# Kernel optimization log

Hardware: AMD Instinct MI355X
Metric: run time of the kernel (lower is better)

## Reference

```python
import jax, jax.numpy as jnp
import numpy as np

COLOR_SIZE = 8
FILTERS = 64
LAYERS = 4
CUMSUM_NORM = 256 * 256 * 3  # hardcoded in original: /256/256/3


def setup_inputs() -> dict:
    key = jax.random.key(0)
    k0, k1, k2, k3 = jax.random.split(key, 4)
    s = 0.05
    example = jax.random.randint(k0, (4, 256, 256, 3), 0, COLOR_SIZE, dtype=jnp.int32)
    # per-channel Dense stacks: layer 0 has input dim 1, layers 1..3 have input dim FILTERS
    W_in_first = jax.random.normal(k1, (3, 1, FILTERS), dtype=jnp.float32) * s
    b_in_first = jnp.zeros((3, FILTERS), dtype=jnp.float32)
    W_in_rest = jax.random.normal(k2, (LAYERS - 1, 3, FILTERS, FILTERS), dtype=jnp.float32) * s
    b_in_rest = jnp.zeros((LAYERS - 1, 3, FILTERS), dtype=jnp.float32)
    W_final = jax.random.normal(k3, (3, FILTERS, COLOR_SIZE), dtype=jnp.float32) * s
    b_final = jnp.zeros((3, COLOR_SIZE), dtype=jnp.float32)
    return {
        "example": example,
        "W_in_first": W_in_first, "b_in_first": b_in_first,
        "W_in_rest": W_in_rest, "b_in_rest": b_in_rest,
        "W_final": W_final, "b_final": b_final,
    }


def reference(example, W_in_first, b_in_first, W_in_rest, b_in_rest, W_final, b_final):
    # example: [B, H, W, 3] int in [0, COLOR_SIZE)
    x = example.astype(jnp.float32) / COLOR_SIZE * 2.0 - 1.0
    B, H, W, _ = x.shape
    L = H * W
    x = x.reshape(B, L, 3, 1)

    def layer(x, Wl, bl):
        # per-channel dense + relu: [B, L, 3, din] x [3, din, dout] -> [B, L, 3, dout]
        x = jax.nn.relu(jnp.einsum('blcd,cde->blce', x, Wl) + bl)
        # flatten channels into the sequence and take causal running sum
        x = x.reshape(B, L * 3, FILTERS)
        x = jnp.cumsum(x, axis=-2) / CUMSUM_NORM
        return x.reshape(B, L, 3, FILTERS)

    x = layer(x, W_in_first, b_in_first)
    for i in range(LAYERS - 1):
        x = layer(x, W_in_rest[i], b_in_rest[i])

    # final per-channel dense to color logits (no activation)
    x = jnp.einsum('blcd,cde->blce', x, W_final) + b_final
    return x.reshape(B, H, W, 3, COLOR_SIZE)
```

## Files before the change

kernel.cpp:

```cpp
#include <hip/hip_runtime.h>
#include <stdint.h>


#define BB 4
#define SP 65536
#define SS 196608
#define CI 1024
#define NG 16
#define INVN (1.0f / 196608.0f)

typedef __attribute__((ext_vector_type(8))) _Float16 half8;
typedef __attribute__((ext_vector_type(4))) float    f32x4;

__global__ __launch_bounds__(256)
void prep(const int* __restrict__ ex, const float* __restrict__ W0,
          const float* __restrict__ b0, const float* __restrict__ Wr,
          const float* __restrict__ Wfin,
          _Float16* __restrict__ Wt16, float* __restrict__ Wd32T,
          _Float16* __restrict__ Wf16p,
          float* __restrict__ Wf32, float* __restrict__ tab32,
          int* __restrict__ Hsub, int* __restrict__ Hgrp)
{
    __shared__ int hist[16][24];
    int tid = threadIdx.x, bi = blockIdx.x;
    int b = bi >> 6, g = (bi >> 2) & 15, q = bi & 3;
    for (int i = tid; i < 384; i += 256) hist[i / 24][i % 24] = 0;
    __syncthreads();
    for (int it = 0; it < 4; ++it) {
        int pl = it * 256 + tid;
        const int* ep = ex + ((size_t)b * SP + g * 4096 + q * 1024 + pl) * 3;
        int j = pl >> 6;
        atomicAdd(&hist[j][ep[0]], 1);
        atomicAdd(&hist[j][8 + ep[1]], 1);
        atomicAdd(&hist[j][16 + ep[2]], 1);
    }
    __syncthreads();
    for (int i = tid; i < 384; i += 256) {
        int j = i / 24, cv = i % 24;
        Hsub[(size_t)(b * CI + g * 64 + q * 16 + j) * 24 + cv] = hist[j][cv];
    }
    if (tid < 24) {
        int s = 0;
        for (int j = 0; j < 16; ++j) s += hist[j][tid];
        atomicAdd(&Hgrp[(size_t)(b * NG + g) * 24 + tid], s);
    }
    {
        int i0 = bi * 256 + tid, nth = 256 * 256;
        for (int idx = i0; idx < 36864; idx += nth) {
            int d = idx & 63, f = (idx >> 6) & 63, lc = idx >> 12;
            float v = Wr[(size_t)(lc * 64 + d) * 64 + f];
            Wt16[idx]  = (_Float16)v;
            Wd32T[idx] = v;
        }
        for (int idx = i0; idx < 3072; idx += nth) {
            int d = idx & 63, n = (idx >> 6) & 15, c = idx >> 10;
            Wf16p[idx] = (n < 8) ? (_Float16)Wfin[(size_t)(c * 64 + d) * 8 + n]
                                 : (_Float16)0.f;
        }
        for (int idx = i0; idx < 1536; idx += nth) {
            int d = idx & 63, ck = idx >> 6;
            Wf32[idx] = Wfin[(size_t)((ck >> 3) * 64 + d) * 8 + (ck & 7)];
        }
        for (int idx = i0; idx < 1536; idx += nth) {
            int f = idx & 63, v = (idx >> 6) & 7, c = idx >> 9;
            float xv = v * 0.25f - 1.0f;
            tab32[idx] = fmaxf(W0[c * 64 + f] * xv + b0[c * 64 + f], 0.f);
        }
    }
}

__global__ __launch_bounds__(256, 4)
void midA(const int* __restrict__ ex,
          const int* __restrict__ Hsub, const int* __restrict__ Hgrp,
          const float* __restrict__ tab32,
          const _Float16* __restrict__ W16, const float* __restrict__ WT32,
          const float* __restrict__ bias, _Float16* __restrict__ Y,
          float* __restrict__ A64, float* __restrict__ Ggrp)
{
    __shared__ float stab[1536];
    __shared__ __align__(16) _Float16 bounce[64 * 72];
    __shared__ float segwt[3][4][64];
    __shared__ float basearr[192];
    __shared__ float hpart[4][24];
    __shared__ float carry[64];

    int tid = threadIdx.x, bi = blockIdx.x;
    int b = bi >> 10, ci = bi & 1023, g = ci >> 6, cr = ci & 63;
    int w = tid >> 6, ln = tid & 63, lm = ln & 15, lq = ln >> 4;
    int P0 = ci * 64;

    for (int i = tid; i < 1536; i += 256) stab[i] = tab32[i];
    if (ln < 24) {
        float s = 0.f;
        for (int j = w; j < g; j += 4)
            s += (float)Hgrp[(size_t)(b * NG + j) * 24 + ln];
        const int* hp = Hsub + (size_t)(b * CI + g * 64) * 24 + ln;
        for (int j = w; j < cr; j += 4) s += (float)hp[j * 24];
        hpart[w][ln] = s;
    }
    __syncthreads();

    float y0[3][16];
    {
#pragma unroll
        for (int p = 0; p < 16; ++p) {
            const int* ep = ex + ((size_t)b * SP + P0 + w * 16 + p) * 3;
            y0[0][p] = stab[ep[0] * 64 + ln];
            y0[1][p] = stab[(8 + ep[1]) * 64 + ln];
            y0[2][p] = stab[(16 + ep[2]) * 64 + ln];
        }
#pragma unroll
        for (int c = 0; c < 3; ++c)
#pragma unroll
            for (int p = 1; p < 16; ++p) y0[c][p] += y0[c][p - 1];
#pragma unroll
        for (int c = 0; c < 3; ++c) segwt[c][w][ln] = y0[c][15];
    }
    if (tid < 64) {
        float c0 = 0.f;
#pragma unroll
        for (int cv = 0; cv < 24; ++cv) {
            float cnt = hpart[0][cv] + hpart[1][cv] + hpart[2][cv] + hpart[3][cv];
            c0 += cnt * stab[cv * 64 + tid];
        }
        carry[tid] = c0;
    }
    __syncthreads();

    float off0[3];
#pragma unroll
    for (int c = 0; c < 3; ++c) {
        float o = 0.f;
        for (int w2 = 0; w2 < w; ++w2) o += segwt[c][w2][ln];
        off0[c] = o;
    }
    if (tid < 192) {
        int c = tid >> 6, f = tid & 63;
        const float* wp = WT32 + (size_t)(c * 64 + f) * 64;
        float a = 0.f;
#pragma unroll 16
        for (int d = 0; d < 64; ++d) a += carry[d] * wp[d];
        basearr[tid] = bias[tid] + INVN * a;
    }

    half8 af0[3], af1[3];
#pragma unroll
    for (int c = 0; c < 3; ++c) {
#pragma unroll
        for (int p = 0; p < 16; ++p) {
            float a0 = y0[0][p] + off0[0];
            float a1 = (c >= 1 ? y0[1][p] : (p ? y0[1][p - 1] : 0.f)) + off0[1];
            float a2 = (c == 2 ? y0[2][p] : (p ? y0[2][p - 1] : 0.f)) + off0[2];
            bounce[(w * 16 + p) * 72 + ln] = (_Float16)(a0 + a1 + a2);
        }
        __syncthreads();
        const half8* bb = (const half8*)bounce;
        af0[c] = bb[(w * 16 + lm) * 9 + lq];
        af1[c] = bb[(w * 16 + lm) * 9 + 4 + lq];
        __syncthreads();
    }

    f32x4 acc[3][4];
#pragma unroll
    for (int c = 0; c < 3; ++c)
#pragma unroll
        for (int nt = 0; nt < 4; ++nt) {
            const half8* bp = (const half8*)(W16 + (size_t)(c * 64 + nt * 16 + lm) * 64);
            f32x4 t = {0.f, 0.f, 0.f, 0.f};
            t = __builtin_amdgcn_mfma_f32_16x16x32_f16(af0[c], bp[lq],     t, 0, 0, 0);
            t = __builtin_amdgcn_mfma_f32_16x16x32_f16(af1[c], bp[4 + lq], t, 0, 0, 0);
            acc[c][nt] = t;
        }

    float s[3][4][4], wexcl[3][4];
#pragma unroll
    for (int c = 0; c < 3; ++c)
#pragma unroll
        for (int nt = 0; nt < 4; ++nt) {
            float base = basearr[c * 64 + nt * 16 + lm];
            float run = 0.f;
#pragma unroll
            for (int r = 0; r < 4; ++r) {
                float yv = fmaxf(base + INVN * acc[c][nt][r], 0.f);
                run += yv; s[c][nt][r] = run;
            }
            float v = run;
            float t1 = __shfl_up(v, 16); if (lq >= 1) v += t1;
            float t2 = __shfl_up(v, 32); if (lq >= 2) v += t2;
            wexcl[c][nt] = v - run;
            if (lq == 3) segwt[c][w][nt * 16 + lm] = v;
        }
    __syncthreads();

    float off[3][4];
    {
        float tot[3][4];
#pragma unroll
        for (int c = 0; c < 3; ++c)
#pragma unroll
            for (int nt = 0; nt < 4; ++nt) {
                float o = wexcl[c][nt], ts = 0.f;
#pragma unroll
                for (int w2 = 0; w2 < 4; ++w2) {
                    float wv = segwt[c][w2][nt * 16 + lm];
                    ts += wv;
                    if (w2 < w) o += wv;
                }
                off[c][nt] = o; tot[c][nt] = ts;
            }
        if (w == 0 && lq == 0)
#pragma unroll
            for (int nt = 0; nt < 4; ++nt) {
                float t3 = tot[0][nt] + tot[1][nt] + tot[2][nt];
                A64[(size_t)(b * CI + ci) * 64 + nt * 16 + lm] = t3;
                atomicAdd(&Ggrp[(size_t)(b * NG + g) * 64 + nt * 16 + lm], t3);
            }
    }

#pragma unroll
    for (int c = 0; c < 3; ++c) {
        if (c) __syncthreads();
#pragma unroll
        for (int nt = 0; nt < 4; ++nt) {
            float offT = off[0][nt] + off[1][nt] + off[2][nt];
#pragma unroll
            for (int r = 0; r < 4; ++r) {
                float s1p = r ? s[1][nt][r - 1] : 0.f;
                float s2p = r ? s[2][nt][r - 1] : 0.f;
                float V = offT + s[0][nt][r];
                float ov = (c == 0) ? (V + s1p + s2p)
                         : (c == 1) ? (V + s[1][nt][r] + s2p)
                                    : (V + s[1][nt][r] + s[2][nt][r]);
                bounce[(w * 16 + lq * 4 + r) * 72 + nt * 16 + lm] = (_Float16)ov;
            }
        }
        __syncthreads();
        const half8* bb = (const half8*)bounce;
        _Float16* Yc = Y + ((size_t)(b * 3 + c) * SP + P0) * 64;
#pragma unroll
        for (int q = 0; q < 2; ++q) {
            int idx = q * 256 + tid;
            int pix = idx >> 3, f8 = idx & 7;
            ((half8*)(Yc + (size_t)pix * 64))[f8] = bb[pix * 9 + f8];
        }
    }
}

__global__ __launch_bounds__(256, 4)
void midB(const _Float16* Yin, _Float16* Yout,
          const float* __restrict__ A64p, const float* __restrict__ Ggrp_p,
          const _Float16* __restrict__ W16, const float* __restrict__ WT32,
          const float* __restrict__ bias,
          float* __restrict__ A64, float* __restrict__ Ggrp)
{
    __shared__ __align__(16) _Float16 bounce[64 * 72];
    __shared__ float wtop[3][4][64];
    __shared__ float basearr[192];
    __shared__ float cpart[4][64];
    __shared__ float carry[64];

    int tid = threadIdx.x, bi = blockIdx.x;
    int b = bi >> 10, ci = bi & 1023, g = ci >> 6, cr = ci & 63;
    int w = tid >> 6, ln = tid & 63, lm = ln & 15, lq = ln >> 4;
    int P0 = ci * 64;

    half8 af0[3], af1[3];
#pragma unroll
    for (int c = 0; c < 3; ++c) {
        const half8* ap = (const half8*)(Yin + ((size_t)(b * 3 + c) * SP + P0 + w * 16 + lm) * 64);
        af0[c] = ap[lq]; af1[c] = ap[4 + lq];
    }
    {
        float s = 0.f;
        for (int j = w; j < g; j += 4)
            s += Ggrp_p[(size_t)(b * NG + j) * 64 + ln];
        const float* ap = A64p + (size_t)(b * CI + g * 64) * 64 + ln;
        for (int j = w; j < cr; j += 4) s += ap[j * 64];
        cpart[w][ln] = s;
    }

    f32x4 acc[3][4];
#pragma unroll
    for (int c = 0; c < 3; ++c)
#pragma unroll
        for (int nt = 0; nt < 4; ++nt) {
            const half8* bp = (const half8*)(W16 + (size_t)(c * 64 + nt * 16 + lm) * 64);
            f32x4 t = {0.f, 0.f, 0.f, 0.f};
            t = __builtin_amdgcn_mfma_f32_16x16x32_f16(af0[c], bp[lq],     t, 0, 0, 0);
            t = __builtin_amdgcn_mfma_f32_16x16x32_f16(af1[c], bp[4 + lq], t, 0, 0, 0);
            acc[c][nt] = t;
        }
    __syncthreads();
    if (tid < 64)
        carry[tid] = cpart[0][tid] + cpart[1][tid] + cpart[2][tid] + cpart[3][tid];
    __syncthreads();
    if (tid < 192) {
        int c = tid >> 6, f = tid & 63;
        const float* wp = WT32 + (size_t)(c * 64 + f) * 64;
        float a = 0.f;
#pragma unroll 16
        for (int d = 0; d < 64; ++d) a += carry[d] * wp[d];
        basearr[tid] = bias[tid] + INVN * a;
    }
    __syncthreads();

    float s[3][4][4], wexcl[3][4];
#pragma unroll
    for (int c = 0; c < 3; ++c)
#pragma unroll
        for (int nt = 0; nt < 4; ++nt) {
            float base = basearr[c * 64 + nt * 16 + lm];
            float run = 0.f;
#pragma unroll
            for (int r = 0; r < 4; ++r) {
                float yv = fmaxf(base + INVN * acc[c][nt][r], 0.f);
                run += yv; s[c][nt][r] = run;
            }
            float v = run;
            float t1 = __shfl_up(v, 16); if (lq >= 1) v += t1;
            float t2 = __shfl_up(v, 32); if (lq >= 2) v += t2;
            wexcl[c][nt] = v - run;
            if (lq == 3) wtop[c][w][nt * 16 + lm] = v;
        }
    __syncthreads();

    float off[3][4];
    {
        float tot[3][4];
#pragma unroll
        for (int c = 0; c < 3; ++c)
#pragma unroll
            for (int nt = 0; nt < 4; ++nt) {
                float o = wexcl[c][nt], ts = 0.f;
#pragma unroll
                for (int w2 = 0; w2 < 4; ++w2) {
                    float wv = wtop[c][w2][nt * 16 + lm];
                    ts += wv;
                    if (w2 < w) o += wv;
                }
                off[c][nt] = o; tot[c][nt] = ts;
            }
        if (w == 0 && lq == 0)
#pragma unroll
            for (int nt = 0; nt < 4; ++nt) {
                float t3 = tot[0][nt] + tot[1][nt] + tot[2][nt];
                A64[(size_t)(b * CI + ci) * 64 + nt * 16 + lm] = t3;
                atomicAdd(&Ggrp[(size_t)(b * NG + g) * 64 + nt * 16 + lm], t3);
            }
    }

#pragma unroll
    for (int c = 0; c < 3; ++c) {
        if (c) __syncthreads();
#pragma unroll
        for (int nt = 0; nt < 4; ++nt) {
            float offT = off[0][nt] + off[1][nt] + off[2][nt];
#pragma unroll
            for (int r = 0; r < 4; ++r) {
                float s1p = r ? s[1][nt][r - 1] : 0.f;
                float s2p = r ? s[2][nt][r - 1] : 0.f;
                float V = offT + s[0][nt][r];
                float ov = (c == 0) ? (V + s1p + s2p)
                         : (c == 1) ? (V + s[1][nt][r] + s2p)
                                    : (V + s[1][nt][r] + s[2][nt][r]);
                bounce[(w * 16 + lq * 4 + r) * 72 + nt * 16 + lm] = (_Float16)ov;
            }
        }
        __syncthreads();
        const half8* bb = (const half8*)bounce;
        _Float16* Yc = Yout + ((size_t)(b * 3 + c) * SP + P0) * 64;
#pragma unroll
        for (int q = 0; q < 2; ++q) {
            int idx = q * 256 + tid;
            int pix = idx >> 3, f8 = idx & 7;
            ((half8*)(Yc + (size_t)pix * 64))[f8] = bb[pix * 9 + f8];
        }
    }
}

__global__ __launch_bounds__(256, 4)
void midC(const _Float16* __restrict__ Yin,
          const float* __restrict__ A64p, const float* __restrict__ Ggrp_p,
          const _Float16* __restrict__ W16, const float* __restrict__ WT32,
          const float* __restrict__ bias,
          const _Float16* __restrict__ Wf16p, const float* __restrict__ bfin,
          float* __restrict__ out, float* __restrict__ A64, float* __restrict__ Ggrp)
{
    __shared__ __align__(16) _Float16 bounce[64 * 72];
    __shared__ float wtop[3][4][64];
    __shared__ float basearr[192];
    __shared__ float cpart[4][64];
    __shared__ float carry[64];
    __shared__ __align__(16) float outst[64 * 28];

    int tid = threadIdx.x, bi = blockIdx.x;
    int b = bi >> 10, ci = bi & 1023, g = ci >> 6, cr = ci & 63;
    int w = tid >> 6, ln = tid & 63, lm = ln & 15, lq = ln >> 4;
    int P0 = ci * 64;

    half8 af0[3], af1[3];
#pragma unroll
    for (int c = 0; c < 3; ++c) {
        const half8* ap = (const half8*)(Yin + ((size_t)(b * 3 + c) * SP + P0 + w * 16 + lm) * 64);
        af0[c] = ap[lq]; af1[c] = ap[4 + lq];
    }
    {
        float s = 0.f;
        for (int j = w; j < g; j += 4)
            s += Ggrp_p[(size_t)(b * NG + j) * 64 + ln];
        const float* ap = A64p + (size_t)(b * CI + g * 64) * 64 + ln;
        for (int j = w; j < cr; j += 4) s += ap[j * 64];
        cpart[w][ln] = s;
    }

    f32x4 acc[3][4];
#pragma unroll
    for (int c = 0; c < 3; ++c)
#pragma unroll
        for (int nt = 0; nt < 4; ++nt) {
            const half8* bp = (const half8*)(W16 + (size_t)(c * 64 + nt * 16 + lm) * 64);
            f32x4 t = {0.f, 0.f, 0.f, 0.f};
            t = __builtin_amdgcn_mfma_f32_16x16x32_f16(af0[c], bp[lq],     t, 0, 0, 0);
            t = __builtin_amdgcn_mfma_f32_16x16x32_f16(af1[c], bp[4 + lq], t, 0, 0, 0);
            acc[c][nt] = t;
        }
    __syncthreads();
    if (tid < 64)
        carry[tid] = cpart[0][tid] + cpart[1][tid] + cpart[2][tid] + cpart[3][tid];
    __syncthreads();
    if (tid < 192) {
        int c = tid >> 6, f = tid & 63;
        const float* wp = WT32 + (size_t)(c * 64 + f) * 64;
        float a = 0.f;
#pragma unroll 16
        for (int d = 0; d < 64; ++d) a += carry[d] * wp[d];
        basearr[tid] = bias[tid] + INVN * a;
    }
    __syncthreads();

    float s[3][4][4], wexcl[3][4];
#pragma unroll
    for (int c = 0; c < 3; ++c)
#pragma unroll
        for (int nt = 0; nt < 4; ++nt) {
            float base = basearr[c * 64 + nt * 16 + lm];
            float run = 0.f;
#pragma unroll
            for (int r = 0; r < 4; ++r) {
                float yv = fmaxf(base + INVN * acc[c][nt][r], 0.f);
                run += yv; s[c][nt][r] = run;
            }
            float v = run;
            float t1 = __shfl_up(v, 16); if (lq >= 1) v += t1;
            float t2 = __shfl_up(v, 32); if (lq >= 2) v += t2;
            wexcl[c][nt] = v - run;
            if (lq == 3) wtop[c][w][nt * 16 + lm] = v;
        }
    __syncthreads();

    float off[3][4];
    {
        float tot[3][4];
#pragma unroll
        for (int c = 0; c < 3; ++c)
#pragma unroll
            for (int nt = 0; nt < 4; ++nt) {
                float o = wexcl[c][nt], ts = 0.f;
#pragma unroll
                for (int w2 = 0; w2 < 4; ++w2) {
                    float wv = wtop[c][w2][nt * 16 + lm];
                    ts += wv;
                    if (w2 < w) o += wv;
                }
                off[c][nt] = o; tot[c][nt] = ts;
            }
        if (w == 0 && lq == 0)
#pragma unroll
            for (int nt = 0; nt < 4; ++nt) {
                float t3 = tot[0][nt] + tot[1][nt] + tot[2][nt];
                A64[(size_t)(b * CI + ci) * 64 + nt * 16 + lm] = t3;
                atomicAdd(&Ggrp[(size_t)(b * NG + g) * 64 + nt * 16 + lm], t3);
            }
    }

#pragma unroll
    for (int c = 0; c < 3; ++c) {
        if (c) __syncthreads();
#pragma unroll
        for (int nt = 0; nt < 4; ++nt) {
            float offT = off[0][nt] + off[1][nt] + off[2][nt];
#pragma unroll
            for (int r = 0; r < 4; ++r) {
                float s1p = r ? s[1][nt][r - 1] : 0.f;
                float s2p = r ? s[2][nt][r - 1] : 0.f;
                float V = offT + s[0][nt][r];
                float ov = (c == 0) ? (V + s1p + s2p)
                         : (c == 1) ? (V + s[1][nt][r] + s2p)
                                    : (V + s[1][nt][r] + s[2][nt][r]);
                bounce[(w * 16 + lq * 4 + r) * 72 + nt * 16 + lm] = (_Float16)ov;
            }
        }
        __syncthreads();
        const half8* bb = (const half8*)bounce;
        half8 fa0 = bb[(w * 16 + lm) * 9 + lq];
        half8 fa1 = bb[(w * 16 + lm) * 9 + 4 + lq];
        const half8* fb = (const half8*)(Wf16p + (size_t)(c * 16 + lm) * 64);
        f32x4 t = {0.f, 0.f, 0.f, 0.f};
        t = __builtin_amdgcn_mfma_f32_16x16x32_f16(fa0, fb[lq],     t, 0, 0, 0);
        t = __builtin_amdgcn_mfma_f32_16x16x32_f16(fa1, fb[4 + lq], t, 0, 0, 0);
        if (lm < 8) {
            float bz = bfin[c * 8 + lm];
#pragma unroll
            for (int r = 0; r < 4; ++r)
                outst[(w * 16 + lq * 4 + r) * 28 + c * 8 + lm] = bz + INVN * t[r];
        }
    }
    __syncthreads();
    {
        float4* obase = (float4*)(out + ((size_t)b * SS + (size_t)P0 * 3) * 8);
#pragma unroll
        for (int k = 0; k < 2; ++k) {
            int idx = k * 256 + tid;
            if (idx < 384) {
                int pix = idx / 6, sub = (idx % 6) * 4;
                obase[idx] = *(const float4*)&outst[pix * 28 + sub];
            }
        }
    }
}

__global__ __launch_bounds__(256, 4)
void fixk(const float* __restrict__ A64p, const float* __restrict__ Ggrp_p,
          const float* __restrict__ Wf32, float* __restrict__ out)
{
    __shared__ float cpart[4][64];
    __shared__ float carry[64];
    __shared__ float part[24][8];
    __shared__ float vfix[24];
    int tid = threadIdx.x, bi = blockIdx.x;
    int b = bi >> 10, ci = bi & 1023, g = ci >> 6, cr = ci & 63;
    int w = tid >> 6, ln = tid & 63;
    int P0 = ci * 64;

    {
        float s = 0.f;
        for (int j = w; j < g; j += 4)
            s += Ggrp_p[(size_t)(b * NG + j) * 64 + ln];
        const float* ap = A64p + (size_t)(b * CI + g * 64) * 64 + ln;
        for (int j = w; j < cr; j += 4) s += ap[j * 64];
        cpart[w][ln] = s;
    }
    __syncthreads();
    if (tid < 64)
        carry[tid] = cpart[0][tid] + cpart[1][tid] + cpart[2][tid] + cpart[3][tid];
    __syncthreads();
    if (tid < 192) {
        int ck = tid >> 3, sg = tid & 7;
        const float* wp = Wf32 + ck * 64 + sg * 8;
        const float* cp = carry + sg * 8;
        float vf = 0.f;
#pragma unroll
        for (int d = 0; d < 8; ++d) vf += cp[d] * wp[d];
        part[ck][sg] = vf;
    }
    __syncthreads();
    if (tid < 24) {
        float vf = 0.f;
#pragma unroll
        for (int j = 0; j < 8; ++j) vf += part[tid][j];
        vfix[tid] = INVN * vf;
    }
    __syncthreads();
    float4* obase = (float4*)(out + ((size_t)b * SS + (size_t)P0 * 3) * 8);
#pragma unroll
    for (int k = 0; k < 2; ++k) {
        int idx = k * 256 + tid;
        if (idx < 384) {
            int sub = (idx % 6) * 4;
            float4 v = obase[idx];
            v.x += vfix[sub];
            v.y += vfix[sub + 1];
            v.z += vfix[sub + 2];
            v.w += vfix[sub + 3];
            obase[idx] = v;
        }
    }
}

extern "C" void kernel_launch(void* const* d_in, const int* in_sizes, int n_in,
                              void* d_out, int out_size, void* d_ws, size_t ws_size,
                              hipStream_t stream)
{
    const int*   ex   = (const int*)d_in[0];
    const float* W0   = (const float*)d_in[1];
    const float* b0   = (const float*)d_in[2];
    const float* Wr   = (const float*)d_in[3];
    const float* br   = (const float*)d_in[4];
    const float* Wfin = (const float*)d_in[5];
    const float* bfin = (const float*)d_in[6];
    float* out = (float*)d_out;

    char* ws = (char*)d_ws;
    size_t off = 0;
    _Float16* Y = (_Float16*)(ws + off); off += (size_t)BB * 3 * SP * 64 * 2;
    float* Ggrp1 = (float*)(ws + off); off += (size_t)BB * NG * 64 * 4;
    float* Ggrp2 = (float*)(ws + off); off += (size_t)BB * NG * 64 * 4;
    float* Ggrp3 = (float*)(ws + off); off += (size_t)BB * NG * 64 * 4;
    float* A64_1 = (float*)(ws + off); off += (size_t)BB * CI * 64 * 4;
    float* A64_2 = (float*)(ws + off); off += (size_t)BB * CI * 64 * 4;
    float* A64_3 = (float*)(ws + off); off += (size_t)BB * CI * 64 * 4;
    int* Hsub = (int*)(ws + off); off += (size_t)BB * CI * 24 * 4;
    int* Hgrp = (int*)(ws + off); off += (size_t)BB * NG * 24 * 4;
    _Float16* Wt16  = (_Float16*)(ws + off); off += 36864 * 2;
    float* Wd32T = (float*)(ws + off); off += 36864 * 4;
    _Float16* Wf16p = (_Float16*)(ws + off); off += 3072 * 2;
    float* Wf32  = (float*)(ws + off); off += 1536 * 4;
    float* tab32 = (float*)(ws + off); off += 1536 * 4;

    hipMemsetAsync(Ggrp1, 0, 3 * (size_t)BB * NG * 64 * 4, stream);
    hipMemsetAsync(Hgrp, 0, (size_t)BB * NG * 24 * 4, stream);
    prep<<<256, 256, 0, stream>>>(ex, W0, b0, Wr, Wfin,
                                  Wt16, Wd32T, Wf16p, Wf32, tab32, Hsub, Hgrp);
    midA<<<4096, 256, 0, stream>>>(ex, Hsub, Hgrp, tab32,
                                   Wt16, Wd32T, br, Y, A64_1, Ggrp1);
    midB<<<4096, 256, 0, stream>>>(Y, Y, A64_1, Ggrp1,
                                   Wt16 + 12288, Wd32T + 12288, br + 192,
                                   A64_2, Ggrp2);
    midC<<<4096, 256, 0, stream>>>(Y, A64_2, Ggrp2,
                                   Wt16 + 24576, Wd32T + 24576, br + 384,
                                   Wf16p, bfin, out, A64_3, Ggrp3);
    fixk<<<4096, 256, 0, stream>>>(A64_3, Ggrp3, Wf32, out);
}
```

Measured before the change: 402.5 us.

## Give each wave its own 64-pixel chunk in midB/midC and batch midA bounce writes

```diff
diff --git a/kernel.cpp b/kernel.cpp
--- a/kernel.cpp
+++ b/kernel.cpp
@@ -11,6 +11,12 @@
 
 typedef __attribute__((ext_vector_type(8))) _Float16 half8;
 typedef __attribute__((ext_vector_type(4))) float    f32x4;
+
+#define WAVE_FENCE() do {                                    \
+    __builtin_amdgcn_sched_barrier(0);                       \
+    asm volatile("s_waitcnt lgkmcnt(0)" ::: "memory");       \
+    __builtin_amdgcn_sched_barrier(0);                       \
+} while (0)
 
 __global__ __launch_bounds__(256)
 void prep(const int* __restrict__ ex, const float* __restrict__ W0,
@@ -78,7 +84,7 @@
           float* __restrict__ A64, float* __restrict__ Ggrp)
 {
     __shared__ float stab[1536];
-    __shared__ __align__(16) _Float16 bounce[64 * 72];
+    __shared__ __align__(16) _Float16 bounce3[3][64 * 72];
     __shared__ float segwt[3][4][64];
     __shared__ float basearr[192];
     __shared__ float hpart[4][24];
@@ -127,12 +133,24 @@
     }
     __syncthreads();
 
-    float off0[3];
-#pragma unroll
-    for (int c = 0; c < 3; ++c) {
-        float o = 0.f;
-        for (int w2 = 0; w2 < w; ++w2) o += segwt[c][w2][ln];
-        off0[c] = o;
+    {
+        float off0[3];
+#pragma unroll
+        for (int c = 0; c < 3; ++c) {
+            float o = 0.f;
+            for (int w2 = 0; w2 < w; ++w2) o += segwt[c][w2][ln];
+            off0[c] = o;
+        }
+#pragma unroll
+        for (int p = 0; p < 16; ++p) {
+            float S0 = y0[0][p] + off0[0], S1 = y0[1][p] + off0[1], S2 = y0[2][p] + off0[2];
+            float P1 = p ? y0[1][p - 1] + off0[1] : off0[1];
+            float P2 = p ? y0[2][p - 1] + off0[2] : off0[2];
+            int row = w * 16 + p;
+            bounce3[0][row * 72 + ln] = (_Float16)(S0 + P1 + P2);
+            bounce3[1][row * 72 + ln] = (_Float16)(S0 + S1 + P2);
+            bounce3[2][row * 72 + ln] = (_Float16)(S0 + S1 + S2);
+        }
     }
     if (tid < 192) {
         int c = tid >> 6, f = tid & 63;
@@ -142,35 +160,23 @@
         for (int d = 0; d < 64; ++d) a += carry[d] * wp[d];
         basearr[tid] = bias[tid] + INVN * a;
     }
-
-    half8 af0[3], af1[3];
+    __syncthreads();
+
+    f32x4 acc[3][4];
 #pragma unroll
     for (int c = 0; c < 3; ++c) {
-#pragma unroll
-        for (int p = 0; p < 16; ++p) {
-            float a0 = y0[0][p] + off0[0];
-            float a1 = (c >= 1 ? y0[1][p] : (p ? y0[1][p - 1] : 0.f)) + off0[1];
-            float a2 = (c == 2 ? y0[2][p] : (p ? y0[2][p - 1] : 0.f)) + off0[2];
-            bounce[(w * 16 + p) * 72 + ln] = (_Float16)(a0 + a1 + a2);
-        }
-        __syncthreads();
-        const half8* bb = (const half8*)bounce;
-        af0[c] = bb[(w * 16 + lm) * 9 + lq];
-        af1[c] = bb[(w * 16 + lm) * 9 + 4 + lq];
-        __syncthreads();
-    }
-
-    f32x4 acc[3][4];
-#pragma unroll
-    for (int c = 0; c < 3; ++c)
+        const half8* bb = (const half8*)&bounce3[c][0];
+        half8 a0 = bb[(w * 16 + lm) * 9 + lq];
+        half8 a1 = bb[(w * 16 + lm) * 9 + 4 + lq];
 #pragma unroll
         for (int nt = 0; nt < 4; ++nt) {
             const half8* bp = (const half8*)(W16 + (size_t)(c * 64 + nt * 16 + lm) * 64);
             f32x4 t = {0.f, 0.f, 0.f, 0.f};
-            t = __builtin_amdgcn_mfma_f32_16x16x32_f16(af0[c], bp[lq],     t, 0, 0, 0);
-            t = __builtin_amdgcn_mfma_f32_16x16x32_f16(af1[c], bp[4 + lq], t, 0, 0, 0);
+            t = __builtin_amdgcn_mfma_f32_16x16x32_f16(a0, bp[lq],     t, 0, 0, 0);
+            t = __builtin_amdgcn_mfma_f32_16x16x32_f16(a1, bp[4 + lq], t, 0, 0, 0);
             acc[c][nt] = t;
         }
+    }
 
     float s[3][4][4], wexcl[3][4];
 #pragma unroll
@@ -192,9 +198,8 @@
         }
     __syncthreads();
 
-    float off[3][4];
-    {
-        float tot[3][4];
+    {
+        float off[3][4], tot[3][4];
 #pragma unroll
         for (int c = 0; c < 3; ++c)
 #pragma unroll
@@ -215,167 +220,168 @@
                 A64[(size_t)(b * CI + ci) * 64 + nt * 16 + lm] = t3;
                 atomicAdd(&Ggrp[(size_t)(b * NG + g) * 64 + nt * 16 + lm], t3);
             }
-    }
-
-#pragma unroll
-    for (int c = 0; c < 3; ++c) {
-        if (c) __syncthreads();
-#pragma unroll
-        for (int nt = 0; nt < 4; ++nt) {
-            float offT = off[0][nt] + off[1][nt] + off[2][nt];
+#pragma unroll
+        for (int nt = 0; nt < 4; ++nt)
 #pragma unroll
             for (int r = 0; r < 4; ++r) {
-                float s1p = r ? s[1][nt][r - 1] : 0.f;
-                float s2p = r ? s[2][nt][r - 1] : 0.f;
-                float V = offT + s[0][nt][r];
-                float ov = (c == 0) ? (V + s1p + s2p)
-                         : (c == 1) ? (V + s[1][nt][r] + s2p)
-                                    : (V + s[1][nt][r] + s[2][nt][r]);
-                bounce[(w * 16 + lq * 4 + r) * 72 + nt * 16 + lm] = (_Float16)ov;
-            }
-        }
-        __syncthreads();
-        const half8* bb = (const half8*)bounce;
-        _Float16* Yc = Y + ((size_t)(b * 3 + c) * SP + P0) * 64;
-#pragma unroll
-        for (int q = 0; q < 2; ++q) {
-            int idx = q * 256 + tid;
-            int pix = idx >> 3, f8 = idx & 7;
-            ((half8*)(Yc + (size_t)pix * 64))[f8] = bb[pix * 9 + f8];
-        }
+                float S0 = off[0][nt] + s[0][nt][r];
+                float S1 = off[1][nt] + s[1][nt][r];
+                float S2 = off[2][nt] + s[2][nt][r];
+                float P1 = off[1][nt] + (r ? s[1][nt][r - 1] : 0.f);
+                float P2 = off[2][nt] + (r ? s[2][nt][r - 1] : 0.f);
+                int row = w * 16 + lq * 4 + r;
+                bounce3[0][row * 72 + nt * 16 + lm] = (_Float16)(S0 + P1 + P2);
+                bounce3[1][row * 72 + nt * 16 + lm] = (_Float16)(S0 + S1 + P2);
+                bounce3[2][row * 72 + nt * 16 + lm] = (_Float16)(S0 + S1 + S2);
+            }
+    }
+    __syncthreads();
+#pragma unroll
+    for (int q = 0; q < 6; ++q) {
+        int idx = q * 256 + tid;
+        int c = idx >> 9, rem = idx & 511;
+        int pix = rem >> 3, f8 = rem & 7;
+        half8 v = *(const half8*)&bounce3[c][pix * 72 + f8 * 8];
+        ((half8*)(Y + ((size_t)(b * 3 + c) * SP + P0 + pix) * 64))[f8] = v;
     }
 }
 
 __global__ __launch_bounds__(256, 4)
-void midB(const _Float16* Yin, _Float16* Yout,
+void midB(const _Float16* __restrict__ Yin, _Float16* __restrict__ Yout,
           const float* __restrict__ A64p, const float* __restrict__ Ggrp_p,
           const _Float16* __restrict__ W16, const float* __restrict__ WT32,
           const float* __restrict__ bias,
           float* __restrict__ A64, float* __restrict__ Ggrp)
 {
-    __shared__ __align__(16) _Float16 bounce[64 * 72];
-    __shared__ float wtop[3][4][64];
-    __shared__ float basearr[192];
     __shared__ float cpart[4][64];
-    __shared__ float carry[64];
+    __shared__ float carry4[4][64];
+    __shared__ float basearr4[4][192];
+    __shared__ __align__(16) _Float16 wb[4][16 * 72];
 
     int tid = threadIdx.x, bi = blockIdx.x;
-    int b = bi >> 10, ci = bi & 1023, g = ci >> 6, cr = ci & 63;
+    int b = bi >> 8, cb = bi & 255;
+    int ci0 = cb * 4, g = cb >> 4, cr0 = ci0 & 63;
     int w = tid >> 6, ln = tid & 63, lm = ln & 15, lq = ln >> 4;
+    int ci = ci0 + w;
     int P0 = ci * 64;
 
-    half8 af0[3], af1[3];
-#pragma unroll
-    for (int c = 0; c < 3; ++c) {
-        const half8* ap = (const half8*)(Yin + ((size_t)(b * 3 + c) * SP + P0 + w * 16 + lm) * 64);
-        af0[c] = ap[lq]; af1[c] = ap[4 + lq];
-    }
     {
         float s = 0.f;
         for (int j = w; j < g; j += 4)
             s += Ggrp_p[(size_t)(b * NG + j) * 64 + ln];
         const float* ap = A64p + (size_t)(b * CI + g * 64) * 64 + ln;
-        for (int j = w; j < cr; j += 4) s += ap[j * 64];
+        for (int j = w; j < cr0; j += 4) s += ap[j * 64];
         cpart[w][ln] = s;
     }
-
-    f32x4 acc[3][4];
-#pragma unroll
-    for (int c = 0; c < 3; ++c)
-#pragma unroll
-        for (int nt = 0; nt < 4; ++nt) {
-            const half8* bp = (const half8*)(W16 + (size_t)(c * 64 + nt * 16 + lm) * 64);
-            f32x4 t = {0.f, 0.f, 0.f, 0.f};
-            t = __builtin_amdgcn_mfma_f32_16x16x32_f16(af0[c], bp[lq],     t, 0, 0, 0);
-            t = __builtin_amdgcn_mfma_f32_16x16x32_f16(af1[c], bp[4 + lq], t, 0, 0, 0);
-            acc[c][nt] = t;
-        }
-    __syncthreads();
-    if (tid < 64)
-        carry[tid] = cpart[0][tid] + cpart[1][tid] + cpart[2][tid] + cpart[3][tid];
+    __syncthreads();
+    {
+        float cw = cpart[0][ln] + cpart[1][ln] + cpart[2][ln] + cpart[3][ln];
+        const float* ap = A64p + (size_t)(b * CI + ci0) * 64 + ln;
+        for (int t = 0; t < w; ++t) cw += ap[t * 64];
+        carry4[w][ln] = cw;
+    }
     __syncthreads();
     if (tid < 192) {
         int c = tid >> 6, f = tid & 63;
         const float* wp = WT32 + (size_t)(c * 64 + f) * 64;
-        float a = 0.f;
-#pragma unroll 16
-        for (int d = 0; d < 64; ++d) a += carry[d] * wp[d];
-        basearr[tid] = bias[tid] + INVN * a;
-    }
-    __syncthreads();
-
-    float s[3][4][4], wexcl[3][4];
+        float a0 = 0.f, a1 = 0.f, a2 = 0.f, a3 = 0.f;
+#pragma unroll 8
+        for (int d = 0; d < 64; ++d) {
+            float wv = wp[d];
+            a0 += carry4[0][d] * wv; a1 += carry4[1][d] * wv;
+            a2 += carry4[2][d] * wv; a3 += carry4[3][d] * wv;
+        }
+        float bz = bias[tid];
+        basearr4[0][tid] = bz + INVN * a0;
+        basearr4[1][tid] = bz + INVN * a1;
+        basearr4[2][tid] = bz + INVN * a2;
+        basearr4[3][tid] = bz + INVN * a3;
+    }
+    __syncthreads();
+
+    float bse[3][4];
 #pragma unroll
     for (int c = 0; c < 3; ++c)
 #pragma unroll
+        for (int nt = 0; nt < 4; ++nt)
+            bse[c][nt] = basearr4[w][c * 64 + nt * 16 + lm];
+    float roff[3][4] = {{0.f,0.f,0.f,0.f},{0.f,0.f,0.f,0.f},{0.f,0.f,0.f,0.f}};
+    _Float16* wbw = &wb[w][0];
+
+#pragma unroll
+    for (int pq = 0; pq < 4; ++pq) {
+        half8 af0[3], af1[3];
+#pragma unroll
+        for (int c = 0; c < 3; ++c) {
+            const half8* ap = (const half8*)(Yin +
+                ((size_t)(b * 3 + c) * SP + P0 + pq * 16 + lm) * 64);
+            af0[c] = ap[lq]; af1[c] = ap[4 + lq];
+        }
+        f32x4 acc[3][4];
+#pragma unroll
+        for (int c = 0; c < 3; ++c)
+#pragma unroll
+            for (int nt = 0; nt < 4; ++nt) {
+                const half8* bp = (const half8*)(W16 + (size_t)(c * 64 + nt * 16 + lm) * 64);
+                f32x4 t = {0.f, 0.f, 0.f, 0.f};
+                t = __builtin_amdgcn_mfma_f32_16x16x32_f16(af0[c], bp[lq],     t, 0, 0, 0);
+                t = __builtin_amdgcn_mfma_f32_16x16x32_f16(af1[c], bp[4 + lq], t, 0, 0, 0);
+                acc[c][nt] = t;
+            }
+
+        float s[3][4][4], off[3][4];
+#pragma unroll
+        for (int c = 0; c < 3; ++c)
+#pragma unroll
+            for (int nt = 0; nt < 4; ++nt) {
+                float base = bse[c][nt];
+                float run = 0.f;
+#pragma unroll
+                for (int r = 0; r < 4; ++r) {
+                    float yv = fmaxf(base + INVN * acc[c][nt][r], 0.f);
+                    run += yv; s[c][nt][r] = run;
+                }
+                float v = run;
+                float t1 = __shfl_up(v, 16); if (lq >= 1) v += t1;
+                float t2 = __shfl_up(v, 32); if (lq >= 2) v += t2;
+                off[c][nt] = roff[c][nt] + (v - run);
+                roff[c][nt] += __shfl(v, 48 + lm);
+            }
+
+#pragma unroll
+        for (int c = 0; c < 3; ++c) {
+#pragma unroll
+            for (int nt = 0; nt < 4; ++nt) {
+                float offT = off[0][nt] + off[1][nt] + off[2][nt];
+#pragma unroll
+                for (int r = 0; r < 4; ++r) {
+                    float s1p = r ? s[1][nt][r - 1] : 0.f;
+                    float s2p = r ? s[2][nt][r - 1] : 0.f;
+                    float V = offT + s[0][nt][r];
+                    float ov = (c == 0) ? (V + s1p + s2p)
+                             : (c == 1) ? (V + s[1][nt][r] + s2p)
+                                        : (V + s[1][nt][r] + s[2][nt][r]);
+                    wbw[(lq * 4 + r) * 72 + nt * 16 + lm] = (_Float16)ov;
+                }
+            }
+            WAVE_FENCE();
+            const half8* bb = (const half8*)wbw;
+            _Float16* Yc = Yout + ((size_t)(b * 3 + c) * SP + P0 + pq * 16) * 64;
+#pragma unroll
+            for (int q = 0; q < 2; ++q) {
+                int idx = q * 64 + ln, pix = idx >> 3, f8 = idx & 7;
+                ((half8*)(Yc + (size_t)pix * 64))[f8] = bb[pix * 9 + f8];
+            }
+        }
+    }
+
+    if (lq == 0)
+#pragma unroll
         for (int nt = 0; nt < 4; ++nt) {
-            float base = basearr[c * 64 + nt * 16 + lm];
-            float run = 0.f;
-#pragma unroll
-            for (int r = 0; r < 4; ++r) {
-                float yv = fmaxf(base + INVN * acc[c][nt][r], 0.f);
-                run += yv; s[c][nt][r] = run;
-            }
-            float v = run;
-            float t1 = __shfl_up(v, 16); if (lq >= 1) v += t1;
-            float t2 = __shfl_up(v, 32); if (lq >= 2) v += t2;
-            wexcl[c][nt] = v - run;
-            if (lq == 3) wtop[c][w][nt * 16 + lm] = v;
-        }
-    __syncthreads();
-
-    float off[3][4];
-    {
-        float tot[3][4];
-#pragma unroll
-        for (int c = 0; c < 3; ++c)
-#pragma unroll
-            for (int nt = 0; nt < 4; ++nt) {
-                float o = wexcl[c][nt], ts = 0.f;
-#pragma unroll
-                for (int w2 = 0; w2 < 4; ++w2) {
-                    float wv = wtop[c][w2][nt * 16 + lm];
-                    ts += wv;
-                    if (w2 < w) o += wv;
-                }
-                off[c][nt] = o; tot[c][nt] = ts;
-            }
-        if (w == 0 && lq == 0)
-#pragma unroll
-            for (int nt = 0; nt < 4; ++nt) {
-                float t3 = tot[0][nt] + tot[1][nt] + tot[2][nt];
-                A64[(size_t)(b * CI + ci) * 64 + nt * 16 + lm] = t3;
-                atomicAdd(&Ggrp[(size_t)(b * NG + g) * 64 + nt * 16 + lm], t3);
-            }
-    }
-
-#pragma unroll
-    for (int c = 0; c < 3; ++c) {
-        if (c) __syncthreads();
-#pragma unroll
-        for (int nt = 0; nt < 4; ++nt) {
-            float offT = off[0][nt] + off[1][nt] + off[2][nt];
-#pragma unroll
-            for (int r = 0; r < 4; ++r) {
-                float s1p = r ? s[1][nt][r - 1] : 0.f;
-                float s2p = r ? s[2][nt][r - 1] : 0.f;
-                float V = offT + s[0][nt][r];
-                float ov = (c == 0) ? (V + s1p + s2p)
-                         : (c == 1) ? (V + s[1][nt][r] + s2p)
-                                    : (V + s[1][nt][r] + s[2][nt][r]);
-                bounce[(w * 16 + lq * 4 + r) * 72 + nt * 16 + lm] = (_Float16)ov;
-            }
-        }
-        __syncthreads();
-        const half8* bb = (const half8*)bounce;
-        _Float16* Yc = Yout + ((size_t)(b * 3 + c) * SP + P0) * 64;
-#pragma unroll
-        for (int q = 0; q < 2; ++q) {
-            int idx = q * 256 + tid;
-            int pix = idx >> 3, f8 = idx & 7;
-            ((half8*)(Yc + (size_t)pix * 64))[f8] = bb[pix * 9 + f8];
-        }
-    }
+            float t3 = roff[0][nt] + roff[1][nt] + roff[2][nt];
+            A64[(size_t)(b * CI + ci) * 64 + nt * 16 + lm] = t3;
+            atomicAdd(&Ggrp[(size_t)(b * NG + g) * 64 + nt * 16 + lm], t3);
+        }
 }
 
 __global__ __launch_bounds__(256, 4)
@@ -386,147 +392,144 @@
           const _Float16* __restrict__ Wf16p, const float* __restrict__ bfin,
           float* __restrict__ out, float* __restrict__ A64, float* __restrict__ Ggrp)
 {
-    __shared__ __align__(16) _Float16 bounce[64 * 72];
-    __shared__ float wtop[3][4][64];
-    __shared__ float basearr[192];
     __shared__ float cpart[4][64];
-    __shared__ float carry[64];
-    __shared__ __align__(16) float outst[64 * 28];
+    __shared__ float carry4[4][64];
+    __shared__ float basearr4[4][192];
+    __shared__ __align__(16) _Float16 wb[4][16 * 72];
 
     int tid = threadIdx.x, bi = blockIdx.x;
-    int b = bi >> 10, ci = bi & 1023, g = ci >> 6, cr = ci & 63;
+    int b = bi >> 8, cb = bi & 255;
+    int ci0 = cb * 4, g = cb >> 4, cr0 = ci0 & 63;
     int w = tid >> 6, ln = tid & 63, lm = ln & 15, lq = ln >> 4;
+    int ci = ci0 + w;
     int P0 = ci * 64;
 
-    half8 af0[3], af1[3];
-#pragma unroll
-    for (int c = 0; c < 3; ++c) {
-        const half8* ap = (const half8*)(Yin + ((size_t)(b * 3 + c) * SP + P0 + w * 16 + lm) * 64);
-        af0[c] = ap[lq]; af1[c] = ap[4 + lq];
-    }
     {
         float s = 0.f;
         for (int j = w; j < g; j += 4)
             s += Ggrp_p[(size_t)(b * NG + j) * 64 + ln];
         const float* ap = A64p + (size_t)(b * CI + g * 64) * 64 + ln;
-        for (int j = w; j < cr; j += 4) s += ap[j * 64];
+        for (int j = w; j < cr0; j += 4) s += ap[j * 64];
         cpart[w][ln] = s;
     }
-
-    f32x4 acc[3][4];
-#pragma unroll
-    for (int c = 0; c < 3; ++c)
-#pragma unroll
-        for (int nt = 0; nt < 4; ++nt) {
-            const half8* bp = (const half8*)(W16 + (size_t)(c * 64 + nt * 16 + lm) * 64);
-            f32x4 t = {0.f, 0.f, 0.f, 0.f};
-            t = __builtin_amdgcn_mfma_f32_16x16x32_f16(af0[c], bp[lq],     t, 0, 0, 0);
-            t = __builtin_amdgcn_mfma_f32_16x16x32_f16(af1[c], bp[4 + lq], t, 0, 0, 0);
-            acc[c][nt] = t;
-        }
-    __syncthreads();
-    if (tid < 64)
-        carry[tid] = cpart[0][tid] + cpart[1][tid] + cpart[2][tid] + cpart[3][tid];
+    __syncthreads();
+    {
+        float cw = cpart[0][ln] + cpart[1][ln] + cpart[2][ln] + cpart[3][ln];
+        const float* ap = A64p + (size_t)(b * CI + ci0) * 64 + ln;
+        for (int t = 0; t < w; ++t) cw += ap[t * 64];
+        carry4[w][ln] = cw;
+    }
     __syncthreads();
     if (tid < 192) {
         int c = tid >> 6, f = tid & 63;
         const float* wp = WT32 + (size_t)(c * 64 + f) * 64;
-        float a = 0.f;
-#pragma unroll 16
-        for (int d = 0; d < 64; ++d) a += carry[d] * wp[d];
-        basearr[tid] = bias[tid] + INVN * a;
-    }
-    __syncthreads();
-
-    float s[3][4][4], wexcl[3][4];
+        float a0 = 0.f, a1 = 0.f, a2 = 0.f, a3 = 0.f;
+#pragma unroll 8
+        for (int d = 0; d < 64; ++d) {
+            float wv = wp[d];
+            a0 += carry4[0][d] * wv; a1 += carry4[1][d] * wv;
+            a2 += carry4[2][d] * wv; a3 += carry4[3][d] * wv;
+        }
+        float bz = bias[tid];
+        basearr4[0][tid] = bz + INVN * a0;
+        basearr4[1][tid] = bz + INVN * a1;
+        basearr4[2][tid] = bz + INVN * a2;
+        basearr4[3][tid] = bz + INVN * a3;
+    }
+    __syncthreads();
+
+    float bse[3][4];
 #pragma unroll
     for (int c = 0; c < 3; ++c)
 #pragma unroll
+        for (int nt = 0; nt < 4; ++nt)
+            bse[c][nt] = basearr4[w][c * 64 + nt * 16 + lm];
+    float roff[3][4] = {{0.f,0.f,0.f,0.f},{0.f,0.f,0.f,0.f},{0.f,0.f,0.f,0.f}};
+    _Float16* wbw = &wb[w][0];
+
+#pragma unroll
+    for (int pq = 0; pq < 4; ++pq) {
+        half8 af0[3], af1[3];
+#pragma unroll
+        for (int c = 0; c < 3; ++c) {
+            const half8* ap = (const half8*)(Yin +
+                ((size_t)(b * 3 + c) * SP + P0 + pq * 16 + lm) * 64);
+            af0[c] = ap[lq]; af1[c] = ap[4 + lq];
+        }
+        f32x4 acc[3][4];
+#pragma unroll
+        for (int c = 0; c < 3; ++c)
+#pragma unroll
+            for (int nt = 0; nt < 4; ++nt) {
+                const half8* bp = (const half8*)(W16 + (size_t)(c * 64 + nt * 16 + lm) * 64);
+                f32x4 t = {0.f, 0.f, 0.f, 0.f};
+                t = __builtin_amdgcn_mfma_f32_16x16x32_f16(af0[c], bp[lq],     t, 0, 0, 0);
+                t = __builtin_amdgcn_mfma_f32_16x16x32_f16(af1[c], bp[4 + lq], t, 0, 0, 0);
+                acc[c][nt] = t;
+            }
+
+        float s[3][4][4], off[3][4];
+#pragma unroll
+        for (int c = 0; c < 3; ++c)
+#pragma unroll
+            for (int nt = 0; nt < 4; ++nt) {
+                float base = bse[c][nt];
+                float run = 0.f;
+#pragma unroll
+                for (int r = 0; r < 4; ++r) {
+                    float yv = fmaxf(base + INVN * acc[c][nt][r], 0.f);
+                    run += yv; s[c][nt][r] = run;
+                }
+                float v = run;
+                float t1 = __shfl_up(v, 16); if (lq >= 1) v += t1;
+                float t2 = __shfl_up(v, 32); if (lq >= 2) v += t2;
+                off[c][nt] = roff[c][nt] + (v - run);
+                roff[c][nt] += __shfl(v, 48 + lm);
+            }
+
+#pragma unroll
+        for (int c = 0; c < 3; ++c) {
+#pragma unroll
+            for (int nt = 0; nt < 4; ++nt) {
+                float offT = off[0][nt] + off[1][nt] + off[2][nt];
+#pragma unroll
+                for (int r = 0; r < 4; ++r) {
+                    float s1p = r ? s[1][nt][r - 1] : 0.f;
+                    float s2p = r ? s[2][nt][r - 1] : 0.f;
+                    float V = offT + s[0][nt][r];
+                    float ov = (c == 0) ? (V + s1p + s2p)
+                             : (c == 1) ? (V + s[1][nt][r] + s2p)
+                                        : (V + s[1][nt][r] + s[2][nt][r]);
+                    wbw[(lq * 4 + r) * 72 + nt * 16 + lm] = (_Float16)ov;
+                }
+            }
+            WAVE_FENCE();
+            const half8* bb = (const half8*)wbw;
+            half8 fa0 = bb[lm * 9 + lq];
+            half8 fa1 = bb[lm * 9 + 4 + lq];
+            const half8* fb = (const half8*)(Wf16p + (size_t)(c * 16 + lm) * 64);
+            f32x4 t = {0.f, 0.f, 0.f, 0.f};
+            t = __builtin_amdgcn_mfma_f32_16x16x32_f16(fa0, fb[lq],     t, 0, 0, 0);
+            t = __builtin_amdgcn_mfma_f32_16x16x32_f16(fa1, fb[4 + lq], t, 0, 0, 0);
+            if (lm < 8) {
+                float bz = bfin[c * 8 + lm];
+                float* ob = out + ((size_t)b * SS +
+                    (size_t)(P0 + pq * 16 + lq * 4) * 3 + c) * 8 + lm;
+#pragma unroll
+                for (int r = 0; r < 4; ++r)
+                    ob[r * 24] = bz + INVN * t[r];
+            }
+            WAVE_FENCE();
+        }
+    }
+
+    if (lq == 0)
+#pragma unroll
         for (int nt = 0; nt < 4; ++nt) {
-            float base = basearr[c * 64 + nt * 16 + lm];
-            float run = 0.f;
-#pragma unroll
-            for (int r = 0; r < 4; ++r) {
-                float yv = fmaxf(base + INVN * acc[c][nt][r], 0.f);
-                run += yv; s[c][nt][r] = run;
-            }
-            float v = run;
-            float t1 = __shfl_up(v, 16); if (lq >= 1) v += t1;
-            float t2 = __shfl_up(v, 32); if (lq >= 2) v += t2;
-            wexcl[c][nt] = v - run;
-            if (lq == 3) wtop[c][w][nt * 16 + lm] = v;
-        }
-    __syncthreads();
-
-    float off[3][4];
-    {
-        float tot[3][4];
-#pragma unroll
-        for (int c = 0; c < 3; ++c)
-#pragma unroll
-            for (int nt = 0; nt < 4; ++nt) {
-                float o = wexcl[c][nt], ts = 0.f;
-#pragma unroll
-                for (int w2 = 0; w2 < 4; ++w2) {
-                    float wv = wtop[c][w2][nt * 16 + lm];
-                    ts += wv;
-                    if (w2 < w) o += wv;
-                }
-                off[c][nt] = o; tot[c][nt] = ts;
-            }
-        if (w == 0 && lq == 0)
-#pragma unroll
-            for (int nt = 0; nt < 4; ++nt) {
-                float t3 = tot[0][nt] + tot[1][nt] + tot[2][nt];
-                A64[(size_t)(b * CI + ci) * 64 + nt * 16 + lm] = t3;
-                atomicAdd(&Ggrp[(size_t)(b * NG + g) * 64 + nt * 16 + lm], t3);
-            }
-    }
-
-#pragma unroll
-    for (int c = 0; c < 3; ++c) {
-        if (c) __syncthreads();
-#pragma unroll
-        for (int nt = 0; nt < 4; ++nt) {
-            float offT = off[0][nt] + off[1][nt] + off[2][nt];
-#pragma unroll
-            for (int r = 0; r < 4; ++r) {
-                float s1p = r ? s[1][nt][r - 1] : 0.f;
-                float s2p = r ? s[2][nt][r - 1] : 0.f;
-                float V = offT + s[0][nt][r];
-                float ov = (c == 0) ? (V + s1p + s2p)
-                         : (c == 1) ? (V + s[1][nt][r] + s2p)
-                                    : (V + s[1][nt][r] + s[2][nt][r]);
-                bounce[(w * 16 + lq * 4 + r) * 72 + nt * 16 + lm] = (_Float16)ov;
-            }
-        }
-        __syncthreads();
-        const half8* bb = (const half8*)bounce;
-        half8 fa0 = bb[(w * 16 + lm) * 9 + lq];
-        half8 fa1 = bb[(w * 16 + lm) * 9 + 4 + lq];
-        const half8* fb = (const half8*)(Wf16p + (size_t)(c * 16 + lm) * 64);
-        f32x4 t = {0.f, 0.f, 0.f, 0.f};
-        t = __builtin_amdgcn_mfma_f32_16x16x32_f16(fa0, fb[lq],     t, 0, 0, 0);
-        t = __builtin_amdgcn_mfma_f32_16x16x32_f16(fa1, fb[4 + lq], t, 0, 0, 0);
-        if (lm < 8) {
-            float bz = bfin[c * 8 + lm];
-#pragma unroll
-            for (int r = 0; r < 4; ++r)
-                outst[(w * 16 + lq * 4 + r) * 28 + c * 8 + lm] = bz + INVN * t[r];
-        }
-    }
-    __syncthreads();
-    {
-        float4* obase = (float4*)(out + ((size_t)b * SS + (size_t)P0 * 3) * 8);
-#pragma unroll
-        for (int k = 0; k < 2; ++k) {
-            int idx = k * 256 + tid;
-            if (idx < 384) {
-                int pix = idx / 6, sub = (idx % 6) * 4;
-                obase[idx] = *(const float4*)&outst[pix * 28 + sub];
-            }
-        }
-    }
+            float t3 = roff[0][nt] + roff[1][nt] + roff[2][nt];
+            A64[(size_t)(b * CI + ci) * 64 + nt * 16 + lm] = t3;
+            atomicAdd(&Ggrp[(size_t)(b * NG + g) * 64 + nt * 16 + lm], t3);
+        }
 }
 
 __global__ __launch_bounds__(256, 4)
@@ -623,10 +626,10 @@
                                   Wt16, Wd32T, Wf16p, Wf32, tab32, Hsub, Hgrp);
     midA<<<4096, 256, 0, stream>>>(ex, Hsub, Hgrp, tab32,
                                    Wt16, Wd32T, br, Y, A64_1, Ggrp1);
-    midB<<<4096, 256, 0, stream>>>(Y, Y, A64_1, Ggrp1,
+    midB<<<1024, 256, 0, stream>>>(Y, Y, A64_1, Ggrp1,
                                    Wt16 + 12288, Wd32T + 12288, br + 192,
                                    A64_2, Ggrp2);
-    midC<<<4096, 256, 0, stream>>>(Y, A64_2, Ggrp2,
+    midC<<<1024, 256, 0, stream>>>(Y, A64_2, Ggrp2,
                                    Wt16 + 24576, Wd32T + 24576, br + 384,
                                    Wf16p, bfin, out, A64_3, Ggrp3);
     fixk<<<4096, 256, 0, stream>>>(A64_3, Ggrp3, Wf32, out);
```

After: 374.8 us. 1.07x faster.
